# Kernel tuning notes

Hardware: AMD Instinct MI355X
Metric: run time of the kernel (lower is better)

## Reference

```python
import jax, jax.numpy as jnp
import numpy as np


def setup_inputs() -> dict:
    key = jax.random.key(0)
    k1, k2 = jax.random.split(key)
    hidden_states = jax.random.normal(k1, (4, 4096, 2048), dtype=jnp.float32)
    routing_params = jax.random.normal(k2, (3, 2048), dtype=jnp.float32)
    return {"hidden_states": hidden_states, "routing_params": routing_params}


def reference(hidden_states, routing_params):
    B, S, H = hidden_states.shape
    D = routing_params.shape[0]  # max_recursion_depth
    k = max(1, int(S * (1.0 / D)))  # top-k tokens selected per step

    depth_assignments = jnp.zeros((B, S), dtype=jnp.int32)
    active_mask = jnp.ones((B, S), dtype=bool)
    rows = jnp.arange(B)[:, None]  # [B,1] row indices for scatter
    scores_list = []

    for r in range(D):  # small fixed depth loop
        raw = jnp.einsum('bsh,h->bs', hidden_states, routing_params[r])
        sc = jax.nn.sigmoid(raw)
        scores_list.append(sc)
        masked = jnp.where(active_mask, sc, -jnp.inf)
        _, top_idx = jax.lax.top_k(masked, k)  # [B,k]
        depth_assignments = depth_assignments.at[rows, top_idx].set(r + 1)
        step_mask = jnp.zeros((B, S), dtype=bool).at[rows, top_idx].set(True)
        active_mask = active_mask & step_mask

    depth_assignments = jnp.where(depth_assignments == 0, 1, depth_assignments)

    # balancing loss: note the original applies sigmoid AGAIN to the already-sigmoided scores
    probs = jax.nn.sigmoid(jnp.stack(scores_list, axis=-1)).mean(axis=(0, 1))  # [D]
    target = jnp.ones_like(probs) / D
    # F.kl_div(probs.log(), target, reduction='batchmean') with input of size D
    balancing_loss = jnp.sum(target * (jnp.log(target) - jnp.log(probs))) / D

    masks = jnp.stack([jnp.ones_like(active_mask) if r == 0 else active_mask
                       for r in range(D)])  # [D,B,S] bool
    return depth_assignments, balancing_loss, masks
```

## Files before the change

### kernel.cpp

```cpp
#include <hip/hip_runtime.h>
#include <hip/hip_bf16.h>
#include <math.h>

namespace {
constexpr int B = 4;
constexpr int S = 4096;
constexpr int H = 2048;
constexpr int DR = 3;
constexpr int KSEL = 1365;
constexpr int NBLK1 = 2048;
constexpr unsigned FONE = 0x3F800000u;
}

__global__ __launch_bounds__(256) void ecr_scores(const float* __restrict__ hid,
                                                  const float* __restrict__ w,
                                                  unsigned* __restrict__ keys,
                                                  float* __restrict__ partials) {
    __shared__ float wl[DR * H];
    __shared__ float s2l[4][DR];
    const float4* wg4 = reinterpret_cast<const float4*>(w);
    float4* wl4 = reinterpret_cast<float4*>(wl);
    for (int i = threadIdx.x; i < DR * H / 4; i += 256) wl4[i] = wg4[i];
    __syncthreads();

    const int wave = threadIdx.x >> 6;
    const int lane = threadIdx.x & 63;
    const int gw = blockIdx.x * 4 + wave;
    const int t0 = gw * 2;
    const float4* wl4_0 = reinterpret_cast<const float4*>(wl);
    const float4* wl4_1 = wl4_0 + (H / 4);
    const float4* wl4_2 = wl4_0 + 2 * (H / 4);
    const float4* h40 = reinterpret_cast<const float4*>(hid) + (size_t)t0 * (H / 4);
    const float4* h41 = h40 + (H / 4);

    float a00 = 0.f, a01 = 0.f, a02 = 0.f;
    float a10 = 0.f, a11 = 0.f, a12 = 0.f;
#pragma unroll
    for (int j = 0; j < H / 256; ++j) {
        const int idx = j * 64 + lane;
        const float4 hv0 = h40[idx];
        const float4 hv1 = h41[idx];
        const float4 w0 = wl4_0[idx];
        const float4 w1 = wl4_1[idx];
        const float4 w2 = wl4_2[idx];
        a00 = fmaf(hv0.x, w0.x, a00); a10 = fmaf(hv1.x, w0.x, a10);
        a00 = fmaf(hv0.y, w0.y, a00); a10 = fmaf(hv1.y, w0.y, a10);
        a00 = fmaf(hv0.z, w0.z, a00); a10 = fmaf(hv1.z, w0.z, a10);
        a00 = fmaf(hv0.w, w0.w, a00); a10 = fmaf(hv1.w, w0.w, a10);
        a01 = fmaf(hv0.x, w1.x, a01); a11 = fmaf(hv1.x, w1.x, a11);
        a01 = fmaf(hv0.y, w1.y, a01); a11 = fmaf(hv1.y, w1.y, a11);
        a01 = fmaf(hv0.z, w1.z, a01); a11 = fmaf(hv1.z, w1.z, a11);
        a01 = fmaf(hv0.w, w1.w, a01); a11 = fmaf(hv1.w, w1.w, a11);
        a02 = fmaf(hv0.x, w2.x, a02); a12 = fmaf(hv1.x, w2.x, a12);
        a02 = fmaf(hv0.y, w2.y, a02); a12 = fmaf(hv1.y, w2.y, a12);
        a02 = fmaf(hv0.z, w2.z, a02); a12 = fmaf(hv1.z, w2.z, a12);
        a02 = fmaf(hv0.w, w2.w, a02); a12 = fmaf(hv1.w, w2.w, a12);
    }
#pragma unroll
    for (int off = 32; off >= 1; off >>= 1) {
        a00 += __shfl_xor(a00, off); a01 += __shfl_xor(a01, off);
        a02 += __shfl_xor(a02, off); a10 += __shfl_xor(a10, off);
        a11 += __shfl_xor(a11, off); a12 += __shfl_xor(a12, off);
    }
    float part0 = 0.f, part1 = 0.f, part2 = 0.f;
    if (lane == 0) {
        const float s00 = 1.0f / (1.0f + expf(-a00));
        const float s01 = 1.0f / (1.0f + expf(-a01));
        const float s02 = 1.0f / (1.0f + expf(-a02));
        const float s10 = 1.0f / (1.0f + expf(-a10));
        const float s11 = 1.0f / (1.0f + expf(-a11));
        const float s12 = 1.0f / (1.0f + expf(-a12));
        keys[t0] = __float_as_uint(s00);
        keys[t0 + 1] = __float_as_uint(s10);
        part0 = 1.0f / (1.0f + expf(-s00)) + 1.0f / (1.0f + expf(-s10));
        part1 = 1.0f / (1.0f + expf(-s01)) + 1.0f / (1.0f + expf(-s11));
        part2 = 1.0f / (1.0f + expf(-s02)) + 1.0f / (1.0f + expf(-s12));
        s2l[wave][0] = part0; s2l[wave][1] = part1; s2l[wave][2] = part2;
    }
    __syncthreads();
    if (threadIdx.x == 0) {
        float p0 = 0.f, p1 = 0.f, p2 = 0.f;
#pragma unroll
        for (int v = 0; v < 4; ++v) { p0 += s2l[v][0]; p1 += s2l[v][1]; p2 += s2l[v][2]; }
        partials[blockIdx.x * 3 + 0] = p0;
        partials[blockIdx.x * 3 + 1] = p1;
        partials[blockIdx.x * 3 + 2] = p2;
    }
}

__global__ __launch_bounds__(512) void ecr_select(const unsigned* __restrict__ keys,
                                                  const float* __restrict__ partials,
                                                  float* __restrict__ out) {
    const int b = blockIdx.x;
    const int t = threadIdx.x;
    const int wave = t >> 6;
    const int lane = t & 63;

    __shared__ int wsum[2][8];
    __shared__ int wscan[8];

    const uint4* kp = reinterpret_cast<const uint4*>(keys + b * S + t * 8);
    const uint4 ka = kp[0], kb = kp[1];
    unsigned kr[8] = {ka.x, ka.y, ka.z, ka.w, kb.x, kb.y, kb.z, kb.w};

    int c = 0;
#pragma unroll
    for (int i = 0; i < 8; ++i) c += (kr[i] == FONE);
#pragma unroll
    for (int off = 32; off >= 1; off >>= 1) c += __shfl_xor(c, off);
    if (lane == 0) wsum[0][wave] = c;
    __syncthreads();
    int tot1 = 0;
#pragma unroll
    for (int w = 0; w < 8; ++w) tot1 += wsum[0][w];

    unsigned vstar;
    int m;
    if (tot1 >= KSEL) {
        vstar = FONE;
        m = KSEL;
    } else {
        unsigned v = 0;
        int pb = 1;
        for (int bit = 29; bit >= 0; --bit) {
            const unsigned cand = v | (1u << bit);
            int cc = 0;
#pragma unroll
            for (int i = 0; i < 8; ++i) cc += (kr[i] >= cand);
#pragma unroll
            for (int off = 32; off >= 1; off >>= 1) cc += __shfl_xor(cc, off);
            if (lane == 0) wsum[pb][wave] = cc;
            __syncthreads();
            int tot = 0;
#pragma unroll
            for (int w = 0; w < 8; ++w) tot += wsum[pb][w];
            if (tot >= KSEL) v = cand;
            pb ^= 1;
        }
        vstar = v;
        int cg = 0;
#pragma unroll
        for (int i = 0; i < 8; ++i) cg += (kr[i] > vstar);
#pragma unroll
        for (int off = 32; off >= 1; off >>= 1) cg += __shfl_xor(cg, off);
        if (lane == 0) wsum[pb][wave] = cg;
        __syncthreads();
        int g = 0;
#pragma unroll
        for (int w = 0; w < 8; ++w) g += wsum[pb][w];
        m = KSEL - g;
    }

    int tc = 0;
#pragma unroll
    for (int i = 0; i < 8; ++i) tc += (kr[i] == vstar);
    int sc = tc;
#pragma unroll
    for (int off = 1; off <= 32; off <<= 1) {
        const int o = __shfl_up(sc, off);
        if (lane >= off) sc += o;
    }
    if (lane == 63) wscan[wave] = sc;
    __syncthreads();
    int wbase = 0;
    for (int w = 0; w < wave; ++w) wbase += wscan[w];
    int rank = wbase + (sc - tc);

    float dep[8], f1[8];
#pragma unroll
    for (int i = 0; i < 8; ++i) {
        int sel;
        if (kr[i] > vstar) sel = 1;
        else if (kr[i] == vstar) { sel = (rank < m) ? 1 : 0; ++rank; }
        else sel = 0;
        dep[i] = sel ? 3.0f : 1.0f;
        f1[i] = sel ? 1.0f : 0.0f;
    }
    float* depth = out;
    float* masks = out + B * S + 1;
    float4* dp4 = reinterpret_cast<float4*>(depth + b * S + t * 8);
    dp4[0] = make_float4(dep[0], dep[1], dep[2], dep[3]);
    dp4[1] = make_float4(dep[4], dep[5], dep[6], dep[7]);
    const int mb = b * S + t * 8;
#pragma unroll
    for (int i = 0; i < 8; ++i) {
        masks[0 * B * S + mb + i] = 1.0f;
        masks[1 * B * S + mb + i] = f1[i];
        masks[2 * B * S + mb + i] = f1[i];
    }

    if (b == 0) {
        __shared__ double red[3][8];
        double a0 = 0.0, a1 = 0.0, a2 = 0.0;
        for (int i = t; i < NBLK1; i += 512) {
            a0 += (double)partials[i * 3 + 0];
            a1 += (double)partials[i * 3 + 1];
            a2 += (double)partials[i * 3 + 2];
        }
#pragma unroll
        for (int off = 32; off >= 1; off >>= 1) {
            a0 += __shfl_xor(a0, off);
            a1 += __shfl_xor(a1, off);
            a2 += __shfl_xor(a2, off);
        }
        if (lane == 0) { red[0][wave] = a0; red[1][wave] = a1; red[2][wave] = a2; }
        __syncthreads();
        if (t == 0) {
            double s0 = 0.0, s1 = 0.0, s2 = 0.0;
#pragma unroll
            for (int w = 0; w < 8; ++w) { s0 += red[0][w]; s1 += red[1][w]; s2 += red[2][w]; }
            const double n = (double)(B * S);
            const double lt = log(1.0 / 3.0);
            double l = (lt - log(s0 / n)) + (lt - log(s1 / n)) + (lt - log(s2 / n));
            out[B * S] = (float)(l * (1.0 / 3.0) / 3.0);
        }
    }
}

extern "C" void kernel_launch(void* const* d_in, const int* in_sizes, int n_in,
                              void* d_out, int out_size, void* d_ws, size_t ws_size,
                              hipStream_t stream) {
    const float* hid = (const float*)d_in[0];
    const float* w   = (const float*)d_in[1];
    float* out = (float*)d_out;

    unsigned* keys  = (unsigned*)d_ws;
    float* partials = (float*)((char*)d_ws + (size_t)B * S * sizeof(unsigned));

    ecr_scores<<<NBLK1, 256, 0, stream>>>(hid, w, keys, partials);
    ecr_select<<<B, 512, 0, stream>>>(keys, partials, out);
}
```

Before: 35.96 us.

## Drop LDS weight staging, use nontemporal hidden loads and per-wave partials

```diff
diff --git a/kernel.cpp b/kernel.cpp
--- a/kernel.cpp
+++ b/kernel.cpp
@@ -9,40 +9,33 @@
 constexpr int DR = 3;
 constexpr int KSEL = 1365;
 constexpr int NBLK1 = 2048;
+constexpr int NWAVE = NBLK1 * 4;
 constexpr unsigned FONE = 0x3F800000u;
-}
-
-__global__ __launch_bounds__(256) void ecr_scores(const float* __restrict__ hid,
-                                                  const float* __restrict__ w,
-                                                  unsigned* __restrict__ keys,
-                                                  float* __restrict__ partials) {
-    __shared__ float wl[DR * H];
-    __shared__ float s2l[4][DR];
-    const float4* wg4 = reinterpret_cast<const float4*>(w);
-    float4* wl4 = reinterpret_cast<float4*>(wl);
-    for (int i = threadIdx.x; i < DR * H / 4; i += 256) wl4[i] = wg4[i];
-    __syncthreads();
-
+typedef float fx4 __attribute__((ext_vector_type(4)));
+}
+
+__global__ __launch_bounds__(256, 4) void ecr_scores(const float* __restrict__ hid,
+                                                     const float* __restrict__ w,
+                                                     unsigned* __restrict__ keys,
+                                                     float* __restrict__ partials) {
     const int wave = threadIdx.x >> 6;
     const int lane = threadIdx.x & 63;
     const int gw = blockIdx.x * 4 + wave;
     const int t0 = gw * 2;
-    const float4* wl4_0 = reinterpret_cast<const float4*>(wl);
-    const float4* wl4_1 = wl4_0 + (H / 4);
-    const float4* wl4_2 = wl4_0 + 2 * (H / 4);
-    const float4* h40 = reinterpret_cast<const float4*>(hid) + (size_t)t0 * (H / 4);
-    const float4* h41 = h40 + (H / 4);
+    const fx4* w4 = reinterpret_cast<const fx4*>(w);
+    const fx4* h40 = reinterpret_cast<const fx4*>(hid) + (size_t)t0 * (H / 4);
+    const fx4* h41 = h40 + (H / 4);
 
     float a00 = 0.f, a01 = 0.f, a02 = 0.f;
     float a10 = 0.f, a11 = 0.f, a12 = 0.f;
 #pragma unroll
-    for (int j = 0; j < H / 256; ++j) {
+    for (int j = 0; j < 8; ++j) {
         const int idx = j * 64 + lane;
-        const float4 hv0 = h40[idx];
-        const float4 hv1 = h41[idx];
-        const float4 w0 = wl4_0[idx];
-        const float4 w1 = wl4_1[idx];
-        const float4 w2 = wl4_2[idx];
+        const fx4 hv0 = __builtin_nontemporal_load(h40 + idx);
+        const fx4 hv1 = __builtin_nontemporal_load(h41 + idx);
+        const fx4 w0 = w4[idx];
+        const fx4 w1 = w4[idx + H / 4];
+        const fx4 w2 = w4[idx + H / 2];
         a00 = fmaf(hv0.x, w0.x, a00); a10 = fmaf(hv1.x, w0.x, a10);
         a00 = fmaf(hv0.y, w0.y, a00); a10 = fmaf(hv1.y, w0.y, a10);
         a00 = fmaf(hv0.z, w0.z, a00); a10 = fmaf(hv1.z, w0.z, a10);
@@ -62,7 +55,6 @@
         a02 += __shfl_xor(a02, off); a10 += __shfl_xor(a10, off);
         a11 += __shfl_xor(a11, off); a12 += __shfl_xor(a12, off);
     }
-    float part0 = 0.f, part1 = 0.f, part2 = 0.f;
     if (lane == 0) {
         const float s00 = 1.0f / (1.0f + expf(-a00));
         const float s01 = 1.0f / (1.0f + expf(-a01));
@@ -70,21 +62,13 @@
         const float s10 = 1.0f / (1.0f + expf(-a10));
         const float s11 = 1.0f / (1.0f + expf(-a11));
         const float s12 = 1.0f / (1.0f + expf(-a12));
-        keys[t0] = __float_as_uint(s00);
-        keys[t0 + 1] = __float_as_uint(s10);
-        part0 = 1.0f / (1.0f + expf(-s00)) + 1.0f / (1.0f + expf(-s10));
-        part1 = 1.0f / (1.0f + expf(-s01)) + 1.0f / (1.0f + expf(-s11));
-        part2 = 1.0f / (1.0f + expf(-s02)) + 1.0f / (1.0f + expf(-s12));
-        s2l[wave][0] = part0; s2l[wave][1] = part1; s2l[wave][2] = part2;
-    }
-    __syncthreads();
-    if (threadIdx.x == 0) {
-        float p0 = 0.f, p1 = 0.f, p2 = 0.f;
-#pragma unroll
-        for (int v = 0; v < 4; ++v) { p0 += s2l[v][0]; p1 += s2l[v][1]; p2 += s2l[v][2]; }
-        partials[blockIdx.x * 3 + 0] = p0;
-        partials[blockIdx.x * 3 + 1] = p1;
-        partials[blockIdx.x * 3 + 2] = p2;
+        uint2 kk;
+        kk.x = __float_as_uint(s00);
+        kk.y = __float_as_uint(s10);
+        *reinterpret_cast<uint2*>(keys + t0) = kk;
+        partials[0 * NWAVE + gw] = 1.0f / (1.0f + expf(-s00)) + 1.0f / (1.0f + expf(-s10));
+        partials[1 * NWAVE + gw] = 1.0f / (1.0f + expf(-s01)) + 1.0f / (1.0f + expf(-s11));
+        partials[2 * NWAVE + gw] = 1.0f / (1.0f + expf(-s02)) + 1.0f / (1.0f + expf(-s12));
     }
 }
 
@@ -191,11 +175,15 @@
 
     if (b == 0) {
         __shared__ double red[3][8];
+        const float4* p4 = reinterpret_cast<const float4*>(partials);
         double a0 = 0.0, a1 = 0.0, a2 = 0.0;
-        for (int i = t; i < NBLK1; i += 512) {
-            a0 += (double)partials[i * 3 + 0];
-            a1 += (double)partials[i * 3 + 1];
-            a2 += (double)partials[i * 3 + 2];
+        for (int i = t; i < NWAVE / 4; i += 512) {
+            const float4 v0 = p4[i];
+            const float4 v1 = p4[NWAVE / 4 + i];
+            const float4 v2 = p4[NWAVE / 2 + i];
+            a0 += (double)v0.x + (double)v0.y + (double)v0.z + (double)v0.w;
+            a1 += (double)v1.x + (double)v1.y + (double)v1.z + (double)v1.w;
+            a2 += (double)v2.x + (double)v2.y + (double)v2.z + (double)v2.w;
         }
 #pragma unroll
         for (int off = 32; off >= 1; off >>= 1) {
```

Result: slower. 37.46 us (+4.2%).

## Coalesce select-kernel accesses, move ones-mask fill to scores kernel, transpose partials

Applied to the files above, without the earlier changes.

```diff
diff --git a/kernel.cpp b/kernel.cpp
--- a/kernel.cpp
+++ b/kernel.cpp
@@ -1,5 +1,4 @@
 #include <hip/hip_runtime.h>
-#include <hip/hip_bf16.h>
 #include <math.h>
 
 namespace {
@@ -15,7 +14,8 @@
 __global__ __launch_bounds__(256) void ecr_scores(const float* __restrict__ hid,
                                                   const float* __restrict__ w,
                                                   unsigned* __restrict__ keys,
-                                                  float* __restrict__ partials) {
+                                                  float* __restrict__ partials,
+                                                  float* __restrict__ out) {
     __shared__ float wl[DR * H];
     __shared__ float s2l[4][DR];
     const float4* wg4 = reinterpret_cast<const float4*>(w);
@@ -36,7 +36,7 @@
     float a00 = 0.f, a01 = 0.f, a02 = 0.f;
     float a10 = 0.f, a11 = 0.f, a12 = 0.f;
 #pragma unroll
-    for (int j = 0; j < H / 256; ++j) {
+    for (int j = 0; j < 8; ++j) {
         const int idx = j * 64 + lane;
         const float4 hv0 = h40[idx];
         const float4 hv1 = h41[idx];
@@ -62,7 +62,6 @@
         a02 += __shfl_xor(a02, off); a10 += __shfl_xor(a10, off);
         a11 += __shfl_xor(a11, off); a12 += __shfl_xor(a12, off);
     }
-    float part0 = 0.f, part1 = 0.f, part2 = 0.f;
     if (lane == 0) {
         const float s00 = 1.0f / (1.0f + expf(-a00));
         const float s01 = 1.0f / (1.0f + expf(-a01));
@@ -70,22 +69,25 @@
         const float s10 = 1.0f / (1.0f + expf(-a10));
         const float s11 = 1.0f / (1.0f + expf(-a11));
         const float s12 = 1.0f / (1.0f + expf(-a12));
-        keys[t0] = __float_as_uint(s00);
-        keys[t0 + 1] = __float_as_uint(s10);
-        part0 = 1.0f / (1.0f + expf(-s00)) + 1.0f / (1.0f + expf(-s10));
-        part1 = 1.0f / (1.0f + expf(-s01)) + 1.0f / (1.0f + expf(-s11));
-        part2 = 1.0f / (1.0f + expf(-s02)) + 1.0f / (1.0f + expf(-s12));
-        s2l[wave][0] = part0; s2l[wave][1] = part1; s2l[wave][2] = part2;
+        uint2 kk;
+        kk.x = __float_as_uint(s00);
+        kk.y = __float_as_uint(s10);
+        *reinterpret_cast<uint2*>(keys + t0) = kk;
+        s2l[wave][0] = 1.0f / (1.0f + expf(-s00)) + 1.0f / (1.0f + expf(-s10));
+        s2l[wave][1] = 1.0f / (1.0f + expf(-s01)) + 1.0f / (1.0f + expf(-s11));
+        s2l[wave][2] = 1.0f / (1.0f + expf(-s02)) + 1.0f / (1.0f + expf(-s12));
     }
     __syncthreads();
     if (threadIdx.x == 0) {
         float p0 = 0.f, p1 = 0.f, p2 = 0.f;
 #pragma unroll
         for (int v = 0; v < 4; ++v) { p0 += s2l[v][0]; p1 += s2l[v][1]; p2 += s2l[v][2]; }
-        partials[blockIdx.x * 3 + 0] = p0;
-        partials[blockIdx.x * 3 + 1] = p1;
-        partials[blockIdx.x * 3 + 2] = p2;
-    }
+        partials[0 * NBLK1 + blockIdx.x] = p0;
+        partials[1 * NBLK1 + blockIdx.x] = p1;
+        partials[2 * NBLK1 + blockIdx.x] = p2;
+    }
+    if (threadIdx.x < 8)
+        out[B * S + 1 + blockIdx.x * 8 + threadIdx.x] = 1.0f;
 }
 
 __global__ __launch_bounds__(512) void ecr_select(const unsigned* __restrict__ keys,
@@ -99,9 +101,9 @@
     __shared__ int wsum[2][8];
     __shared__ int wscan[8];
 
-    const uint4* kp = reinterpret_cast<const uint4*>(keys + b * S + t * 8);
-    const uint4 ka = kp[0], kb = kp[1];
-    unsigned kr[8] = {ka.x, ka.y, ka.z, ka.w, kb.x, kb.y, kb.z, kb.w};
+    unsigned kr[8];
+#pragma unroll
+    for (int i = 0; i < 8; ++i) kr[i] = keys[b * S + i * 512 + t];
 
     int c = 0;
 #pragma unroll
@@ -112,7 +114,7 @@
     __syncthreads();
     int tot1 = 0;
 #pragma unroll
-    for (int w = 0; w < 8; ++w) tot1 += wsum[0][w];
+    for (int w2 = 0; w2 < 8; ++w2) tot1 += wsum[0][w2];
 
     unsigned vstar;
     int m;
@@ -133,7 +135,7 @@
             __syncthreads();
             int tot = 0;
 #pragma unroll
-            for (int w = 0; w < 8; ++w) tot += wsum[pb][w];
+            for (int w2 = 0; w2 < 8; ++w2) tot += wsum[pb][w2];
             if (tot >= KSEL) v = cand;
             pb ^= 1;
         }
@@ -147,56 +149,59 @@
         __syncthreads();
         int g = 0;
 #pragma unroll
-        for (int w = 0; w < 8; ++w) g += wsum[pb][w];
+        for (int w2 = 0; w2 < 8; ++w2) g += wsum[pb][w2];
         m = KSEL - g;
     }
-
-    int tc = 0;
-#pragma unroll
-    for (int i = 0; i < 8; ++i) tc += (kr[i] == vstar);
-    int sc = tc;
-#pragma unroll
-    for (int off = 1; off <= 32; off <<= 1) {
-        const int o = __shfl_up(sc, off);
-        if (lane >= off) sc += o;
-    }
-    if (lane == 63) wscan[wave] = sc;
-    __syncthreads();
-    int wbase = 0;
-    for (int w = 0; w < wave; ++w) wbase += wscan[w];
-    int rank = wbase + (sc - tc);
-
-    float dep[8], f1[8];
+    __syncthreads();
+
+    int rank[8];
+    int cum = 0;
+    for (int i = 0; i < 8; ++i) {
+        const int tci = (kr[i] == vstar) ? 1 : 0;
+        int sc = tci;
+#pragma unroll
+        for (int off = 1; off <= 32; off <<= 1) {
+            const int o = __shfl_up(sc, off);
+            if (lane >= off) sc += o;
+        }
+        if (lane == 63) wscan[wave] = sc;
+        __syncthreads();
+        int base = 0, tot = 0;
+#pragma unroll
+        for (int w2 = 0; w2 < 8; ++w2) {
+            if (w2 < wave) base += wscan[w2];
+            tot += wscan[w2];
+        }
+        rank[i] = cum + base + (sc - tci);
+        cum += tot;
+        __syncthreads();
+    }
+
+    float* depth  = out;
+    float* masks1 = out + B * S + 1 + 1 * B * S;
+    float* masks2 = out + B * S + 1 + 2 * B * S;
+    const int s0 = b * S + t;
 #pragma unroll
     for (int i = 0; i < 8; ++i) {
         int sel;
         if (kr[i] > vstar) sel = 1;
-        else if (kr[i] == vstar) { sel = (rank < m) ? 1 : 0; ++rank; }
+        else if (kr[i] == vstar) sel = (rank[i] < m) ? 1 : 0;
         else sel = 0;
-        dep[i] = sel ? 3.0f : 1.0f;
-        f1[i] = sel ? 1.0f : 0.0f;
-    }
-    float* depth = out;
-    float* masks = out + B * S + 1;
-    float4* dp4 = reinterpret_cast<float4*>(depth + b * S + t * 8);
-    dp4[0] = make_float4(dep[0], dep[1], dep[2], dep[3]);
-    dp4[1] = make_float4(dep[4], dep[5], dep[6], dep[7]);
-    const int mb = b * S + t * 8;
-#pragma unroll
-    for (int i = 0; i < 8; ++i) {
-        masks[0 * B * S + mb + i] = 1.0f;
-        masks[1 * B * S + mb + i] = f1[i];
-        masks[2 * B * S + mb + i] = f1[i];
+        const float fsel = sel ? 1.0f : 0.0f;
+        depth[s0 + i * 512]  = sel ? 3.0f : 1.0f;
+        masks1[s0 + i * 512] = fsel;
+        masks2[s0 + i * 512] = fsel;
     }
 
     if (b == 0) {
         __shared__ double red[3][8];
-        double a0 = 0.0, a1 = 0.0, a2 = 0.0;
-        for (int i = t; i < NBLK1; i += 512) {
-            a0 += (double)partials[i * 3 + 0];
-            a1 += (double)partials[i * 3 + 1];
-            a2 += (double)partials[i * 3 + 2];
-        }
+        const float4* p4 = reinterpret_cast<const float4*>(partials);
+        const float4 v0 = p4[t];
+        const float4 v1 = p4[NBLK1 / 4 + t];
+        const float4 v2 = p4[NBLK1 / 2 + t];
+        double a0 = (double)v0.x + (double)v0.y + (double)v0.z + (double)v0.w;
+        double a1 = (double)v1.x + (double)v1.y + (double)v1.z + (double)v1.w;
+        double a2 = (double)v2.x + (double)v2.y + (double)v2.z + (double)v2.w;
 #pragma unroll
         for (int off = 32; off >= 1; off >>= 1) {
             a0 += __shfl_xor(a0, off);
@@ -206,12 +211,12 @@
         if (lane == 0) { red[0][wave] = a0; red[1][wave] = a1; red[2][wave] = a2; }
         __syncthreads();
         if (t == 0) {
-            double s0 = 0.0, s1 = 0.0, s2 = 0.0;
-#pragma unroll
-            for (int w = 0; w < 8; ++w) { s0 += red[0][w]; s1 += red[1][w]; s2 += red[2][w]; }
+            double s0d = 0.0, s1d = 0.0, s2d = 0.0;
+#pragma unroll
+            for (int w2 = 0; w2 < 8; ++w2) { s0d += red[0][w2]; s1d += red[1][w2]; s2d += red[2][w2]; }
             const double n = (double)(B * S);
             const double lt = log(1.0 / 3.0);
-            double l = (lt - log(s0 / n)) + (lt - log(s1 / n)) + (lt - log(s2 / n));
+            double l = (lt - log(s0d / n)) + (lt - log(s1d / n)) + (lt - log(s2d / n));
             out[B * S] = (float)(l * (1.0 / 3.0) / 3.0);
         }
     }
@@ -227,6 +232,6 @@
     unsigned* keys  = (unsigned*)d_ws;
     float* partials = (float*)((char*)d_ws + (size_t)B * S * sizeof(unsigned));
 
-    ecr_scores<<<NBLK1, 256, 0, stream>>>(hid, w, keys, partials);
+    ecr_scores<<<NBLK1, 256, 0, stream>>>(hid, w, keys, partials, out);
     ecr_select<<<B, 512, 0, stream>>>(keys, partials, out);
 }
```

New measurement: 37.01 us. 1.03x slower.
